# Performance work log

Hardware: AMD Instinct MI355X
Metric: run time of the kernel (lower is better)

The kernel has to match this reference:

```python
import jax, jax.numpy as jnp
import numpy as np

B, H, W = 4, 192, 448
BWEIGHT = 5.0   # backward_weight for level 3
K, P, DC = 5, 2, 25  # unfold/dist kernel, padding, dist channels


def conv(x, w, b, pad):
    y = jax.lax.conv_general_dilated(x, w, (1, 1), pad,
                                     dimension_numbers=('NCHW', 'OIHW', 'NCHW'))
    return y + b[None, :, None, None]


def lrelu(x):
    return jnp.where(x >= 0, x, 0.1 * x)


def backwarp(img, flow):
    # bilinear backward warp, zero padding, align_corners=True convention
    _, C, h, w = img.shape
    yy, xx = jnp.meshgrid(jnp.arange(h, dtype=img.dtype), jnp.arange(w, dtype=img.dtype), indexing='ij')
    x = xx[None] + flow[:, 0]  # [B,H,W] absolute sample coords
    y = yy[None] + flow[:, 1]
    x0 = jnp.floor(x); y0 = jnp.floor(y)
    wx1 = x - x0; wy1 = y - y0
    wx0 = 1.0 - wx1; wy0 = 1.0 - wy1

    def gather(yi, xi):
        valid = ((yi >= 0) & (yi < h) & (xi >= 0) & (xi < w)).astype(img.dtype)
        yc = jnp.clip(yi, 0, h - 1).astype(jnp.int32)
        xc = jnp.clip(xi, 0, w - 1).astype(jnp.int32)
        v = jax.vmap(lambda im, yv, xv: im[:, yv, xv])(img, yc, xc)  # [B,C,H,W]
        return v * valid[:, None]

    return (gather(y0, x0) * (wy0 * wx0)[:, None] + gather(y0, x0 + 1) * (wy0 * wx1)[:, None]
            + gather(y0 + 1, x0) * (wy1 * wx0)[:, None] + gather(y0 + 1, x0 + 1) * (wy1 * wx1)[:, None])


def unfold1(x):
    # x: [B,1,H,W] -> [B,K*K,H,W], patch order (kh,kw) row-major like torch unfold
    return jax.lax.conv_general_dilated_patches(x, (K, K), (1, 1), ((P, P), (P, P)))


def setup_inputs() -> dict:
    key = jax.random.key(0)
    ks = jax.random.split(key, 24)
    f32 = jnp.float32
    inp = {
        'tensor1': jax.random.normal(ks[0], (B, 3, H, W), f32),
        'tensor2': jax.random.normal(ks[1], (B, 3, H, W), f32),
        'features_tensor1': jax.random.normal(ks[2], (B, 64, H, W), f32),
        'features_tensor2': jax.random.normal(ks[3], (B, 64, H, W), f32),
        'flow_tensor': jax.random.normal(ks[4], (B, 2, H, W), f32) * 2.0,
    }

    def wgt(i, shape):
        fan = int(np.prod(shape[1:]))
        return jax.random.normal(ks[i], shape, f32) / np.sqrt(fan)

    inp['feat_w'] = wgt(5, (128, 64, 1, 1)); inp['feat_b'] = jnp.zeros((128,), f32)
    inp['main_w1'] = wgt(6, (128, 131, 3, 3)); inp['main_b1'] = jnp.zeros((128,), f32)
    inp['main_w2'] = wgt(7, (128, 128, 3, 3)); inp['main_b2'] = jnp.zeros((128,), f32)
    inp['main_w3'] = wgt(8, (64, 128, 3, 3)); inp['main_b3'] = jnp.zeros((64,), f32)
    inp['main_w4'] = wgt(9, (64, 64, 3, 3)); inp['main_b4'] = jnp.zeros((64,), f32)
    inp['main_w5'] = wgt(10, (32, 64, 3, 3)); inp['main_b5'] = jnp.zeros((32,), f32)
    inp['main_w6'] = wgt(11, (32, 32, 3, 3)); inp['main_b6'] = jnp.zeros((32,), f32)
    inp['dist_w1'] = wgt(12, (DC, 32, K, 1)); inp['dist_b1'] = jnp.zeros((DC,), f32)
    inp['dist_w2'] = wgt(13, (DC, DC, 1, K)); inp['dist_b2'] = jnp.zeros((DC,), f32)
    inp['sx_w'] = wgt(14, (1, DC, 1, 1)); inp['sx_b'] = jnp.zeros((1,), f32)
    inp['sy_w'] = wgt(15, (1, DC, 1, 1)); inp['sy_b'] = jnp.zeros((1,), f32)
    return inp


def reference(tensor1, tensor2, features_tensor1, features_tensor2, flow_tensor,
              feat_w, feat_b, main_w1, main_b1, main_w2, main_b2, main_w3, main_b3,
              main_w4, main_b4, main_w5, main_b5, main_w6, main_b6,
              dist_w1, dist_b1, dist_w2, dist_b2, sx_w, sx_b, sy_w, sy_b):
    z = ((0, 0), (0, 0))
    o = ((1, 1), (1, 1))
    warp = backwarp(tensor2, flow_tensor * BWEIGHT)
    diff = jax.lax.stop_gradient(jnp.sqrt(jnp.sum((tensor1 - warp) ** 2, axis=1, keepdims=True)))
    feat = lrelu(conv(features_tensor1, feat_w, feat_b, z))
    flow_c = flow_tensor - jnp.mean(flow_tensor, axis=(2, 3), keepdims=True)
    x = jnp.concatenate([diff, flow_c, feat], axis=1)  # [B,131,H,W]
    for w, b in [(main_w1, main_b1), (main_w2, main_b2), (main_w3, main_b3),
                 (main_w4, main_b4), (main_w5, main_b5), (main_w6, main_b6)]:
        x = lrelu(conv(x, w, b, o))
    dist = conv(x, dist_w1, dist_b1, ((P, P), (0, 0)))   # 5x1 conv
    dist = conv(dist, dist_w2, dist_b2, ((0, 0), (P, P)))  # 1x5 conv
    dist = -(dist * dist)
    dist = jnp.exp(dist - jnp.max(dist, axis=1, keepdims=True))  # [B,25,H,W]
    divisor = 1.0 / jnp.sum(dist, axis=1, keepdims=True)
    u1 = unfold1(flow_tensor[:, 0:1])  # [B,25,H,W]
    u2 = unfold1(flow_tensor[:, 1:2])
    sx = conv(dist * u1, sx_w, sx_b, z) * divisor
    sy = conv(dist * u2, sy_w, sy_b, z) * divisor
    return jnp.concatenate([sx, sy], axis=1)
```

## Files before the change

### kernel.cpp

```cpp
#include <hip/hip_runtime.h>
#include <math.h>

#define HH 192
#define WW 448
#define HW (HH * WW)
#define PW2 450
#define PH2 194
#define NPAD 87300
#define NPADT 87552
#define GUARD 1024
#define NB 4

typedef _Float16 half8 __attribute__((ext_vector_type(8)));
typedef _Float16 half4v __attribute__((ext_vector_type(4)));
typedef float float4v __attribute__((ext_vector_type(4)));

__global__ void mean_kernel(const float* __restrict__ flow, float* __restrict__ means) {
    int bc = blockIdx.x;
    const float* src = flow + (size_t)bc * HW;
    float s = 0.f;
    for (int i = threadIdx.x; i < HW; i += 256) s += src[i];
    __shared__ float red[256];
    red[threadIdx.x] = s;
    __syncthreads();
    for (int off = 128; off > 0; off >>= 1) {
        if (threadIdx.x < off) red[threadIdx.x] += red[threadIdx.x + off];
        __syncthreads();
    }
    if (threadIdx.x == 0) means[bc] = red[0] * (1.0f / (float)HW);
}

__global__ void wtrans_kernel(const float* __restrict__ w, _Float16* __restrict__ wt,
                              int cinReal, int nchunk, int cout, int nshift, int perm,
                              int total) {
    int idx = blockIdx.x * 256 + threadIdx.x;
    if (idx >= total) return;
    int k = idx & 31;
    int r = idx >> 5;
    int m = r % cout;
    int r2 = r / cout;
    int q = r2 % nchunk;
    int s = r2 / nchunk;
    int icb = q * 32 + k;
    float val = 0.f;
    if (perm) {
        if (icb < 131) {
            int icr = (icb < 128) ? icb + 3 : icb - 128;
            val = w[((size_t)m * cinReal + icr) * nshift + s];
        }
    } else if (icb < cinReal) {
        val = w[((size_t)m * cinReal + icb) * nshift + s];
    }
    wt[idx] = (_Float16)val;
}

__global__ void feat_transpose(const float* __restrict__ feat, _Float16* __restrict__ F,
                               size_t fSlot) {
    __shared__ _Float16 tile[64 * 72];
    int t = threadIdx.x;
    int z = blockIdx.y;
    int pix0 = blockIdx.x * 64;
    const float* src = feat + (size_t)z * 64 * HW + pix0;
#pragma unroll
    for (int pass = 0; pass < 16; ++pass) {
        int c = pass * 4 + (t >> 6);
        int pl = t & 63;
        tile[pl * 72 + c] = (_Float16)src[(size_t)c * HW + pl];
    }
    __syncthreads();
    int row = pix0 / WW;
    int xcol = pix0 - row * WW;
    size_t n0 = (size_t)(row + 1) * PW2 + xcol + 1;
    _Float16* dst = F + (size_t)z * fSlot + n0 * 64;
#pragma unroll
    for (int pass = 0; pass < 2; ++pass) {
        int pl = (t >> 3) + pass * 32;
        int seg = t & 7;
        *(half8*)&dst[(size_t)pl * 64 + seg * 8] = *(const half8*)&tile[pl * 72 + seg * 8];
    }
}

__global__ void prep_kernel(const float* __restrict__ t1, const float* __restrict__ t2,
                            const float* __restrict__ flow, const float* __restrict__ means,
                            _Float16* __restrict__ bufA, size_t aSlot) {
    int n = blockIdx.x * 256 + threadIdx.x;
    if (n >= NPAD) return;
    int z = blockIdx.y;
    _Float16* dst = bufA + (size_t)z * aSlot + (size_t)n * 160 + 128;
    int y = n / PW2, x = n - PW2 * y;
    if (y < 1 || y > HH || x < 1 || x > WW) {
        dst[0] = (_Float16)0.f; dst[1] = (_Float16)0.f; dst[2] = (_Float16)0.f;
        return;
    }
    int iy = y - 1, ix = x - 1, pix = iy * WW + ix;
    const float* fb = flow + (size_t)z * 2 * HW;
    float fx = fb[pix];
    float fy = fb[HW + pix];
    float sx = (float)ix + fx * 5.0f;
    float sy = (float)iy + fy * 5.0f;
    float fx0 = floorf(sx), fy0 = floorf(sy);
    float wx1 = sx - fx0, wy1 = sy - fy0;
    float wx0 = 1.f - wx1, wy0 = 1.f - wy1;
    int ix0 = (int)fx0, iy0 = (int)fy0;
    bool y0ok = (iy0 >= 0) && (iy0 < HH);
    bool y1ok = (iy0 + 1 >= 0) && (iy0 + 1 < HH);
    bool x0ok = (ix0 >= 0) && (ix0 < WW);
    bool x1ok = (ix0 + 1 >= 0) && (ix0 + 1 < WW);
    float d2 = 0.f;
    for (int c = 0; c < 3; ++c) {
        const float* img = t2 + ((size_t)z * 3 + c) * HW;
        float v00 = (y0ok && x0ok) ? img[iy0 * WW + ix0] : 0.f;
        float v01 = (y0ok && x1ok) ? img[iy0 * WW + ix0 + 1] : 0.f;
        float v10 = (y1ok && x0ok) ? img[(iy0 + 1) * WW + ix0] : 0.f;
        float v11 = (y1ok && x1ok) ? img[(iy0 + 1) * WW + ix0 + 1] : 0.f;
        float v = v00 * (wy0 * wx0) + v01 * (wy0 * wx1) + v10 * (wy1 * wx0) + v11 * (wy1 * wx1);
        float d = t1[((size_t)z * 3 + c) * HW + pix] - v;
        d2 += d * d;
    }
    dst[0] = (_Float16)sqrtf(d2);
    dst[1] = (_Float16)(fx - means[z * 2 + 0]);
    dst[2] = (_Float16)(fy - means[z * 2 + 1]);
}

template <int BM, int KH, int KW, int CSIN, int NCHUNK, int CSOUT>
__launch_bounds__(256, 4)
__global__ void mfma_conv(const _Float16* __restrict__ in, size_t inSlot,
                          const _Float16* __restrict__ wt,
                          const float* __restrict__ bias,
                          _Float16* __restrict__ out, size_t outSlot) {
    constexpr int MT = BM / 32;
    __shared__ __align__(16) _Float16 Blds[128 * 32];
    const int t = threadIdx.x;
    const int wave = t >> 6, lane = t & 63;
    const int wm = wave >> 1, wn = wave & 1;
    const int col = lane & 15, quad = lane >> 4;
    const int n0 = blockIdx.x * 128;
    const _Float16* inImg = in + (size_t)blockIdx.z * inSlot;
    _Float16* outImg = out + (size_t)blockIdx.z * outSlot;

    const _Float16* dmaBase =
        inImg + (ptrdiff_t)(n0 + wave * 16 + (lane >> 2)) * CSIN + (lane & 3) * 8;
    _Float16* dst0 = &Blds[(wave * 16) * 32];
    _Float16* dst1 = &Blds[(64 + wave * 16) * 32];
    const _Float16* aBase = wt + ((size_t)(wm * MT * 16 + col)) * 32 + quad * 8;

    float4v acc[MT][4];
#pragma unroll
    for (int i = 0; i < MT; ++i)
#pragma unroll
        for (int j = 0; j < 4; ++j) acc[i][j] = float4v{0.f, 0.f, 0.f, 0.f};

#pragma unroll
    for (int s = 0; s < KH * KW; ++s) {
        const int off = (s / KW - KH / 2) * PW2 + (s % KW - KW / 2);
        const _Float16* gs = dmaBase + (ptrdiff_t)off * CSIN;
        const _Float16* as = aBase + (size_t)s * NCHUNK * BM * 32;
#pragma unroll
        for (int q = 0; q < NCHUNK; ++q) {
            __syncthreads();
            __builtin_amdgcn_global_load_lds(
                (const __attribute__((address_space(1))) void*)(gs + q * 32),
                (__attribute__((address_space(3))) void*)dst0, 16, 0, 0);
            __builtin_amdgcn_global_load_lds(
                (const __attribute__((address_space(1))) void*)(gs + q * 32 + 64 * CSIN),
                (__attribute__((address_space(3))) void*)dst1, 16, 0, 0);
            half8 aF[MT];
#pragma unroll
            for (int mt = 0; mt < MT; ++mt)
                aF[mt] = *(const half8*)(as + (size_t)q * BM * 32 + mt * 16 * 32);
            __syncthreads();
            half8 bF[4];
#pragma unroll
            for (int nt = 0; nt < 4; ++nt)
                bF[nt] = *(const half8*)&Blds[(wn * 64 + nt * 16 + col) * 32 + quad * 8];
#pragma unroll
            for (int mt = 0; mt < MT; ++mt)
#pragma unroll
                for (int nt = 0; nt < 4; ++nt)
                    acc[mt][nt] = __builtin_amdgcn_mfma_f32_16x16x32_f16(
                        aF[mt], bF[nt], acc[mt][nt], 0, 0, 0);
        }
    }
#pragma unroll
    for (int mt = 0; mt < MT; ++mt) {
        const int m0 = wm * MT * 16 + mt * 16 + quad * 4;
        float bv[4];
#pragma unroll
        for (int i = 0; i < 4; ++i) bv[i] = bias[m0 + i];
#pragma unroll
        for (int nt = 0; nt < 4; ++nt) {
            int n = n0 + wn * 64 + nt * 16 + col;
            int y = n / PW2, x = n - y * PW2;
            bool ok = (y >= 1) && (y <= HH) && (x >= 1) && (x <= WW) && (n < NPAD);
            half4v h;
#pragma unroll
            for (int i = 0; i < 4; ++i) {
                float v = acc[mt][nt][i] + bv[i];
                v = (v >= 0.f) ? v : 0.1f * v;
                h[i] = ok ? (_Float16)v : (_Float16)0.f;
            }
            *(half4v*)&outImg[(size_t)n * CSOUT + m0] = h;
        }
    }
}

__global__ void dist1_kernel(const _Float16* __restrict__ in, size_t inSlot,
                             const float* __restrict__ w, const float* __restrict__ bias,
                             float* __restrict__ outD, size_t outSlot) {
    __shared__ float wl[25 * 32 * 5];
    int t = threadIdx.x;
    for (int i = t; i < 4000; i += 256) wl[i] = w[i];
    __syncthreads();
    int p = blockIdx.x * 256 + t;
    int z = blockIdx.y;
    const _Float16* inI = in + (size_t)z * inSlot;
    float* out = outD + (size_t)z * outSlot;
    int y = p / WW, x = p - y * WW;
    float acc[25];
#pragma unroll
    for (int oc = 0; oc < 25; ++oc) acc[oc] = bias[oc];
    for (int kh = 0; kh < 5; ++kh) {
        int yy = y + kh - 2;
        if (yy < 0 || yy >= HH) continue;
        const _Float16* src = inI + (size_t)((yy + 1) * PW2 + x + 1) * 32;
        _Float16 vals[32];
#pragma unroll
        for (int g = 0; g < 4; ++g) *(half8*)&vals[g * 8] = *(const half8*)&src[g * 8];
#pragma unroll
        for (int ic = 0; ic < 32; ++ic) {
            float v = (float)vals[ic];
#pragma unroll
            for (int oc = 0; oc < 25; ++oc)
                acc[oc] = fmaf(v, wl[(oc * 32 + ic) * 5 + kh], acc[oc]);
        }
    }
#pragma unroll
    for (int oc = 0; oc < 25; ++oc) out[(size_t)p * 25 + oc] = acc[oc];
}

__global__ void final_kernel(const float* __restrict__ D1, size_t d1Slot,
                             const float* __restrict__ flow,
                             const float* __restrict__ dw2, const float* __restrict__ db2,
                             const float* __restrict__ sxw, const float* __restrict__ sxb,
                             const float* __restrict__ syw, const float* __restrict__ syb,
                             float* __restrict__ out) {
    __shared__ float wl[25 * 25 * 5];
    int t = threadIdx.x;
    for (int i = t; i < 3125; i += 256) wl[i] = dw2[i];
    __syncthreads();
    int p = blockIdx.x * 256 + t;
    int z = blockIdx.y;
    const float* D = D1 + (size_t)z * d1Slot;
    int y = p / WW, x = p - y * WW;
    float acc[25];
#pragma unroll
    for (int oc = 0; oc < 25; ++oc) acc[oc] = db2[oc];
    for (int kw = 0; kw < 5; ++kw) {
        int xx = x + kw - 2;
        if (xx < 0 || xx >= WW) continue;
        const float* src = D + (size_t)(y * WW + xx) * 25;
#pragma unroll
        for (int ic = 0; ic < 25; ++ic) {
            float v = src[ic];
#pragma unroll
            for (int oc = 0; oc < 25; ++oc)
                acc[oc] = fmaf(v, wl[(oc * 25 + ic) * 5 + kw], acc[oc]);
        }
    }
    float e[25];
    float m = -1e30f;
#pragma unroll
    for (int c = 0; c < 25; ++c) {
        float d = -(acc[c] * acc[c]);
        e[c] = d;
        m = fmaxf(m, d);
    }
    float s = 0.f;
#pragma unroll
    for (int c = 0; c < 25; ++c) {
        e[c] = expf(e[c] - m);
        s += e[c];
    }
    const float* f0 = flow + (size_t)z * 2 * HW;
    const float* f1 = f0 + HW;
    float ax = sxb[0], ay = syb[0];
#pragma unroll
    for (int kh = 0; kh < 5; ++kh) {
        int iy = y + kh - 2;
        bool yok = (iy >= 0) && (iy < HH);
#pragma unroll
        for (int kw = 0; kw < 5; ++kw) {
            int ix = x + kw - 2;
            int c = kh * 5 + kw;
            float u1 = 0.f, u2 = 0.f;
            if (yok && ix >= 0 && ix < WW) {
                int q = iy * WW + ix;
                u1 = f0[q];
                u2 = f1[q];
            }
            ax = fmaf(e[c] * u1, sxw[c], ax);
            ay = fmaf(e[c] * u2, syw[c], ay);
        }
    }
    float inv = 1.0f / s;
    out[(size_t)z * 2 * HW + p] = ax * inv;
    out[(size_t)z * 2 * HW + HW + p] = ay * inv;
}

extern "C" void kernel_launch(void* const* d_in, const int* in_sizes, int n_in,
                              void* d_out, int out_size, void* d_ws, size_t ws_size,
                              hipStream_t stream) {
    const float* t1      = (const float*)d_in[0];
    const float* t2      = (const float*)d_in[1];
    const float* feat_in = (const float*)d_in[2];
    const float* flow    = (const float*)d_in[4];
    const float* feat_w  = (const float*)d_in[5];
    const float* feat_b  = (const float*)d_in[6];
    const float* w1 = (const float*)d_in[7];   const float* b1 = (const float*)d_in[8];
    const float* w2 = (const float*)d_in[9];   const float* b2 = (const float*)d_in[10];
    const float* w3 = (const float*)d_in[11];  const float* b3 = (const float*)d_in[12];
    const float* w4 = (const float*)d_in[13];  const float* b4 = (const float*)d_in[14];
    const float* w5 = (const float*)d_in[15];  const float* b5 = (const float*)d_in[16];
    const float* w6 = (const float*)d_in[17];  const float* b6 = (const float*)d_in[18];
    const float* dw1 = (const float*)d_in[19]; const float* db1 = (const float*)d_in[20];
    const float* dw2 = (const float*)d_in[21]; const float* db2 = (const float*)d_in[22];
    const float* sxw = (const float*)d_in[23]; const float* sxb = (const float*)d_in[24];
    const float* syw = (const float*)d_in[25]; const float* syb = (const float*)d_in[26];
    float* out = (float*)d_out;
    char* ws = (char*)d_ws;

    const size_t OFF_FEAT = 0;
    const size_t OFF_C1 = 8192;
    const size_t OFF_C2 = 192512;
    const size_t OFF_C3 = 339968;
    const size_t OFF_C4 = 413696;
    const size_t OFF_C5 = 450560;
    const size_t OFF_C6 = 468992;
    const size_t WT_BYTES = 478208 * 2;

    _Float16* wt = (_Float16*)ws;
    float* means = (float*)(ws + WT_BYTES);
    const size_t F0 = WT_BYTES + 64;
    const size_t F_SLOT_B = (size_t)(NPADT + 2 * GUARD) * 64 * 2;
    const size_t A_SLOT_B = (size_t)(NPADT + 2 * GUARD) * 160 * 2;
    const size_t B_SLOT_B = (size_t)(NPADT + 2 * GUARD) * 128 * 2;
    const size_t C_SLOT_B = B_SLOT_B;
    const size_t PER_IMG = F_SLOT_B + A_SLOT_B + B_SLOT_B + C_SLOT_B;
    const size_t needFull = F0 + NB * PER_IMG;
    const int step = (ws_size >= needFull) ? NB : 1;

    const size_t A0 = F0 + step * F_SLOT_B;
    const size_t B0 = A0 + step * A_SLOT_B;
    const size_t C0 = B0 + step * B_SLOT_B;

    _Float16* Fd    = (_Float16*)(ws + F0) + (size_t)GUARD * 64;
    _Float16* Ad    = (_Float16*)(ws + A0) + (size_t)GUARD * 160;
    _Float16* Bd128 = (_Float16*)(ws + B0) + (size_t)GUARD * 128;
    _Float16* Bd64  = (_Float16*)(ws + B0) + (size_t)GUARD * 64;
    _Float16* Bd32  = (_Float16*)(ws + B0) + (size_t)GUARD * 32;
    _Float16* Cd128 = (_Float16*)(ws + C0) + (size_t)GUARD * 128;
    _Float16* Cd64  = (_Float16*)(ws + C0) + (size_t)GUARD * 64;
    _Float16* Cd32  = (_Float16*)(ws + C0) + (size_t)GUARD * 32;
    float* D1 = (float*)(ws + F0);

    const size_t FSL = F_SLOT_B / 2, ASL = A_SLOT_B / 2, BSL = B_SLOT_B / 2,
                 CSL = C_SLOT_B / 2, DSL = F_SLOT_B / 4;

    mean_kernel<<<8, 256, 0, stream>>>(flow, means);

    auto wlaunch = [&](const float* src, size_t dst, int cin, int nch, int cout,
                       int nsh, int perm) {
        int total = nsh * nch * cout * 32;
        wtrans_kernel<<<(total + 255) / 256, 256, 0, stream>>>(
            src, wt + dst, cin, nch, cout, nsh, perm, total);
    };
    wlaunch(feat_w, OFF_FEAT, 64, 2, 128, 1, 0);
    wlaunch(w1, OFF_C1, 131, 5, 128, 9, 1);
    wlaunch(w2, OFF_C2, 128, 4, 128, 9, 0);
    wlaunch(w3, OFF_C3, 128, 4, 64, 9, 0);
    wlaunch(w4, OFF_C4, 64, 2, 64, 9, 0);
    wlaunch(w5, OFF_C5, 64, 2, 32, 9, 0);
    wlaunch(w6, OFF_C6, 32, 1, 32, 9, 0);

    const int NT = NPADT / 128;

    for (int b0 = 0; b0 < NB; b0 += step) {
        dim3 gconv(NT, 1, step);
        feat_transpose<<<dim3(HW / 64, step), 256, 0, stream>>>(
            feat_in + (size_t)b0 * 64 * HW, Fd, FSL);
        prep_kernel<<<dim3((NPAD + 255) / 256, step), 256, 0, stream>>>(
            t1 + (size_t)b0 * 3 * HW, t2 + (size_t)b0 * 3 * HW,
            flow + (size_t)b0 * 2 * HW, means + b0 * 2, Ad, ASL);
        mfma_conv<128, 1, 1, 64, 2, 160><<<gconv, 256, 0, stream>>>(
            Fd, FSL, wt + OFF_FEAT, feat_b, Ad, ASL);
        mfma_conv<128, 3, 3, 160, 5, 128><<<gconv, 256, 0, stream>>>(
            Ad, ASL, wt + OFF_C1, b1, Bd128, BSL);
        mfma_conv<128, 3, 3, 128, 4, 128><<<gconv, 256, 0, stream>>>(
            Bd128, BSL, wt + OFF_C2, b2, Cd128, CSL);
        mfma_conv<64, 3, 3, 128, 4, 64><<<gconv, 256, 0, stream>>>(
            Cd128, CSL, wt + OFF_C3, b3, Bd64, BSL);
        mfma_conv<64, 3, 3, 64, 2, 64><<<gconv, 256, 0, stream>>>(
            Bd64, BSL, wt + OFF_C4, b4, Cd64, CSL);
        mfma_conv<32, 3, 3, 64, 2, 32><<<gconv, 256, 0, stream>>>(
            Cd64, CSL, wt + OFF_C5, b5, Bd32, BSL);
        mfma_conv<32, 3, 3, 32, 1, 32><<<gconv, 256, 0, stream>>>(
            Bd32, BSL, wt + OFF_C6, b6, Cd32, CSL);
        dist1_kernel<<<dim3(HW / 256, step), 256, 0, stream>>>(
            Cd32, CSL, dw1, db1, D1, DSL);
        final_kernel<<<dim3(HW / 256, step), 256, 0, stream>>>(
            D1, DSL, flow + (size_t)b0 * 2 * HW, dw2, db2, sxw, sxb, syw, syb,
            out + (size_t)b0 * 2 * HW);
    }
}
```

Measured before the change: 1.248 ms.

## Stage full-channel row strips with halo in LDS to reuse across 3x3 taps

The conv kernel no longer reloads a 32-channel slice from global memory for every tap and chunk with two barriers each. It now loads a strip of BN+2 pixels with all input channels per kernel row into LDS, then reuses it across the three horizontal taps and all channel chunks. The change also adds a configurable wave layout (wider 256-pixel tiles for the 32-channel layers) and a block-index swizzle into 8 bands with an early exit for padded blocks. LDS use per block grows with CSIN, which may lower occupancy, and the unswizzled row-major LDS reads may cause bank conflicts.

```diff
diff --git a/kernel.cpp b/kernel.cpp
--- a/kernel.cpp
+++ b/kernel.cpp
@@ -122,27 +122,37 @@
     dst[2] = (_Float16)(fy - means[z * 2 + 1]);
 }
 
-template <int BM, int KH, int KW, int CSIN, int NCHUNK, int CSOUT>
+template <int BM, int WN, int K3, int CSIN, int NCHUNK, int CSOUT>
 __launch_bounds__(256, 4)
 __global__ void mfma_conv(const _Float16* __restrict__ in, size_t inSlot,
                           const _Float16* __restrict__ wt,
                           const float* __restrict__ bias,
-                          _Float16* __restrict__ out, size_t outSlot) {
-    constexpr int MT = BM / 32;
-    __shared__ __align__(16) _Float16 Blds[128 * 32];
+                          _Float16* __restrict__ out, size_t outSlot, int NT) {
+    constexpr int WM = 4 / WN;
+    constexpr int MT = BM / (16 * WM);
+    constexpr int BN = WN * 64;
+    constexpr int HALO = K3 ? 2 : 0;
+    constexpr int NSTG = K3 ? 3 : 1;
+    constexpr int NSH = K3 ? 3 : 1;
+    constexpr int NISSUE = (( (BN + HALO) * CSIN * 2) + 4095) / 4096;
+    __shared__ __align__(16) _Float16 Blds[NISSUE * 2048];
+
     const int t = threadIdx.x;
     const int wave = t >> 6, lane = t & 63;
-    const int wm = wave >> 1, wn = wave & 1;
+    const int wm = wave / WN, wn = wave % WN;
     const int col = lane & 15, quad = lane >> 4;
-    const int n0 = blockIdx.x * 128;
+
+    const int band = (int)(gridDim.x >> 3);
+    const int sblk = (blockIdx.x & 7) * band + (blockIdx.x >> 3);
+    if (sblk >= NT) return;
+    const int n0 = sblk * BN;
+
     const _Float16* inImg = in + (size_t)blockIdx.z * inSlot;
     _Float16* outImg = out + (size_t)blockIdx.z * outSlot;
 
-    const _Float16* dmaBase =
-        inImg + (ptrdiff_t)(n0 + wave * 16 + (lane >> 2)) * CSIN + (lane & 3) * 8;
-    _Float16* dst0 = &Blds[(wave * 16) * 32];
-    _Float16* dst1 = &Blds[(64 + wave * 16) * 32];
     const _Float16* aBase = wt + ((size_t)(wm * MT * 16 + col)) * 32 + quad * 8;
+    const _Float16* strip0 = inImg + (ptrdiff_t)(n0 - (K3 ? 1 : 0)) * CSIN;
+    const int local = wn * 64 + col;
 
     float4v acc[MT][4];
 #pragma unroll
@@ -151,34 +161,38 @@
         for (int j = 0; j < 4; ++j) acc[i][j] = float4v{0.f, 0.f, 0.f, 0.f};
 
 #pragma unroll
-    for (int s = 0; s < KH * KW; ++s) {
-        const int off = (s / KW - KH / 2) * PW2 + (s % KW - KW / 2);
-        const _Float16* gs = dmaBase + (ptrdiff_t)off * CSIN;
-        const _Float16* as = aBase + (size_t)s * NCHUNK * BM * 32;
-#pragma unroll
-        for (int q = 0; q < NCHUNK; ++q) {
-            __syncthreads();
+    for (int stg = 0; stg < NSTG; ++stg) {
+        const _Float16* src = strip0 + (ptrdiff_t)(stg - (K3 ? 1 : 0)) * PW2 * CSIN;
+        __syncthreads();
+#pragma unroll
+        for (int j = 0; j < NISSUE; ++j)
             __builtin_amdgcn_global_load_lds(
-                (const __attribute__((address_space(1))) void*)(gs + q * 32),
-                (__attribute__((address_space(3))) void*)dst0, 16, 0, 0);
-            __builtin_amdgcn_global_load_lds(
-                (const __attribute__((address_space(1))) void*)(gs + q * 32 + 64 * CSIN),
-                (__attribute__((address_space(3))) void*)dst1, 16, 0, 0);
-            half8 aF[MT];
-#pragma unroll
-            for (int mt = 0; mt < MT; ++mt)
-                aF[mt] = *(const half8*)(as + (size_t)q * BM * 32 + mt * 16 * 32);
-            __syncthreads();
-            half8 bF[4];
-#pragma unroll
-            for (int nt = 0; nt < 4; ++nt)
-                bF[nt] = *(const half8*)&Blds[(wn * 64 + nt * 16 + col) * 32 + quad * 8];
-#pragma unroll
-            for (int mt = 0; mt < MT; ++mt)
+                (const __attribute__((address_space(1))) void*)(src + (j * 256 + t) * 8),
+                (__attribute__((address_space(3))) void*)&Blds[(j * 256 + wave * 64) * 8],
+                16, 0, 0);
+        __syncthreads();
+#pragma unroll
+        for (int dx = 0; dx < NSH; ++dx) {
+            const int s = K3 ? (stg * 3 + dx) : 0;
+            const _Float16* as = aBase + (size_t)s * NCHUNK * BM * 32;
+#pragma unroll
+            for (int q = 0; q < NCHUNK; ++q) {
+                half8 aF[MT];
+#pragma unroll
+                for (int mt = 0; mt < MT; ++mt)
+                    aF[mt] = *(const half8*)(as + (size_t)q * BM * 32 + mt * 512);
+                half8 bF[4];
 #pragma unroll
                 for (int nt = 0; nt < 4; ++nt)
-                    acc[mt][nt] = __builtin_amdgcn_mfma_f32_16x16x32_f16(
-                        aF[mt], bF[nt], acc[mt][nt], 0, 0, 0);
+                    bF[nt] = *(const half8*)&Blds[((K3 ? dx : 0) + local + nt * 16) * CSIN +
+                                                  q * 32 + quad * 8];
+#pragma unroll
+                for (int mt = 0; mt < MT; ++mt)
+#pragma unroll
+                    for (int nt = 0; nt < 4; ++nt)
+                        acc[mt][nt] = __builtin_amdgcn_mfma_f32_16x16x32_f16(
+                            aF[mt], bF[nt], acc[mt][nt], 0, 0, 0);
+            }
         }
     }
 #pragma unroll
@@ -382,29 +396,31 @@
     wlaunch(w5, OFF_C5, 64, 2, 32, 9, 0);
     wlaunch(w6, OFF_C6, 32, 1, 32, 9, 0);
 
-    const int NT = NPADT / 128;
+    const int NT128 = NPADT / 128;
+    const int NT256 = NPADT / 256;
+    const int NTP128 = 688;
+    const int NTP256 = 344;
 
     for (int b0 = 0; b0 < NB; b0 += step) {
-        dim3 gconv(NT, 1, step);
         feat_transpose<<<dim3(HW / 64, step), 256, 0, stream>>>(
             feat_in + (size_t)b0 * 64 * HW, Fd, FSL);
         prep_kernel<<<dim3((NPAD + 255) / 256, step), 256, 0, stream>>>(
             t1 + (size_t)b0 * 3 * HW, t2 + (size_t)b0 * 3 * HW,
             flow + (size_t)b0 * 2 * HW, means + b0 * 2, Ad, ASL);
-        mfma_conv<128, 1, 1, 64, 2, 160><<<gconv, 256, 0, stream>>>(
-            Fd, FSL, wt + OFF_FEAT, feat_b, Ad, ASL);
-        mfma_conv<128, 3, 3, 160, 5, 128><<<gconv, 256, 0, stream>>>(
-            Ad, ASL, wt + OFF_C1, b1, Bd128, BSL);
-        mfma_conv<128, 3, 3, 128, 4, 128><<<gconv, 256, 0, stream>>>(
-            Bd128, BSL, wt + OFF_C2, b2, Cd128, CSL);
-        mfma_conv<64, 3, 3, 128, 4, 64><<<gconv, 256, 0, stream>>>(
-            Cd128, CSL, wt + OFF_C3, b3, Bd64, BSL);
-        mfma_conv<64, 3, 3, 64, 2, 64><<<gconv, 256, 0, stream>>>(
-            Bd64, BSL, wt + OFF_C4, b4, Cd64, CSL);
-        mfma_conv<32, 3, 3, 64, 2, 32><<<gconv, 256, 0, stream>>>(
-            Cd64, CSL, wt + OFF_C5, b5, Bd32, BSL);
-        mfma_conv<32, 3, 3, 32, 1, 32><<<gconv, 256, 0, stream>>>(
-            Bd32, BSL, wt + OFF_C6, b6, Cd32, CSL);
+        mfma_conv<128, 2, 0, 64, 2, 160><<<dim3(NTP128, 1, step), 256, 0, stream>>>(
+            Fd, FSL, wt + OFF_FEAT, feat_b, Ad, ASL, NT128);
+        mfma_conv<128, 2, 1, 160, 5, 128><<<dim3(NTP128, 1, step), 256, 0, stream>>>(
+            Ad, ASL, wt + OFF_C1, b1, Bd128, BSL, NT128);
+        mfma_conv<128, 2, 1, 128, 4, 128><<<dim3(NTP128, 1, step), 256, 0, stream>>>(
+            Bd128, BSL, wt + OFF_C2, b2, Cd128, CSL, NT128);
+        mfma_conv<64, 2, 1, 128, 4, 64><<<dim3(NTP128, 1, step), 256, 0, stream>>>(
+            Cd128, CSL, wt + OFF_C3, b3, Bd64, BSL, NT128);
+        mfma_conv<64, 2, 1, 64, 2, 64><<<dim3(NTP128, 1, step), 256, 0, stream>>>(
+            Bd64, BSL, wt + OFF_C4, b4, Cd64, CSL, NT128);
+        mfma_conv<32, 4, 1, 64, 2, 32><<<dim3(NTP256, 1, step), 256, 0, stream>>>(
+            Cd64, CSL, wt + OFF_C5, b5, Bd32, BSL, NT256);
+        mfma_conv<32, 4, 1, 32, 1, 32><<<dim3(NTP256, 1, step), 256, 0, stream>>>(
+            Bd32, BSL, wt + OFF_C6, b6, Cd32, CSL, NT256);
         dist1_kernel<<<dim3(HW / 256, step), 256, 0, stream>>>(
             Cd32, CSL, dw1, db1, D1, DSL);
         final_kernel<<<dim3(HW / 256, step), 256, 0, stream>>>(
```

After: 1.106 ms. 1.13x faster.
